# Kernel optimization log

Measured on AMD Instinct MI355X. Metric: run time of the kernel, lower is better.

Reference implementation:

```python
import jax, jax.numpy as jnp
import numpy as np

N, E = 50000, 800000
H_IN, H, L = 256, 128, 3
EPS = 1e-5  # BatchNorm1d default eps


def setup_inputs() -> dict:
    key = jax.random.key(0)
    ks = jax.random.split(key, 8)
    x = jax.random.normal(ks[0], (N, H_IN), jnp.float32)
    edge_index = jax.random.randint(ks[1], (2, E), 0, N, dtype=jnp.int32)

    def glorot(k, fi, fo):
        lim = np.sqrt(6.0 / (fi + fo)).astype(np.float32)
        return jax.random.uniform(k, (fi, fo), jnp.float32, -lim, lim)

    W_feat = glorot(ks[2], H_IN, H)
    b_feat = jnp.zeros((H,), jnp.float32)
    wkeys = jax.random.split(ks[3], L)
    Ws = jnp.stack([glorot(wkeys[i], H, H) for i in range(L)])
    bs = jnp.zeros((L, H), jnp.float32)
    # BN init per reset_parameters: weight=1, bias=1e-4
    bn_feat_g = jnp.ones((H_IN,), jnp.float32)
    bn_feat_b = jnp.full((H_IN,), 1e-4, jnp.float32)
    bn_g = jnp.ones((L, H), jnp.float32)
    bn_b = jnp.full((L, H), 1e-4, jnp.float32)
    return dict(x=x, edge_index=edge_index, bn_feat_g=bn_feat_g, bn_feat_b=bn_feat_b,
                W_feat=W_feat, b_feat=b_feat, bn_g=bn_g, bn_b=bn_b, Ws=Ws, bs=bs)


def _bn(x, gamma, beta):
    # training-mode BatchNorm1d: batch statistics over nodes, biased variance
    mu = x.mean(0)
    var = x.var(0)
    return (x - mu) * jax.lax.rsqrt(var + EPS) * gamma + beta


def _gcn_norm(edge_index, n):
    # add self-loops (fill value 1) + symmetric deg^-1/2 normalization
    row, col = edge_index[0], edge_index[1]
    loop = jnp.arange(n, dtype=row.dtype)
    row = jnp.concatenate([row, loop])
    col = jnp.concatenate([col, loop])
    deg = jax.ops.segment_sum(jnp.ones_like(row, jnp.float32), row, num_segments=n)
    dinv = jnp.where(deg > 0, jax.lax.rsqrt(deg), 0.0)
    return row, col, dinv[row] * dinv[col]


def _gcn(x, W, b, row, col, norm, n):
    x = x @ W                                   # [n, out]
    msg = x[row] * norm[:, None]                # gather + scale, [E+n, out]
    out = jax.ops.segment_sum(msg, col, num_segments=n)  # scatter-add
    return out + b


def reference(x, edge_index, bn_feat_g, bn_feat_b, W_feat, b_feat, bn_g, bn_b, Ws, bs):
    n = x.shape[0]
    row, col, norm = _gcn_norm(edge_index, n)   # same for every layer
    x = _bn(x, bn_feat_g, bn_feat_b)
    x = _gcn(x, W_feat, b_feat, row, col, norm, n)
    for i in range(L):
        x = _bn(x, bn_g[i], bn_b[i])
        x = _gcn(x, Ws[i], bs[i], row, col, norm, n)
    return x
```

## Files before the change

kernel.cpp:

```cpp
#include <hip/hip_runtime.h>
#include <hip/hip_bf16.h>

#define H_IN 256
#define H    128
#define BN_EPS 1e-5f
#define NCOPY 32
#define NSLICE 256
#define HSL 64
#define SMAX 5120
#define STATS_FLOATS (NCOPY * 2 * H_IN)
#define SBLK 1024
#define GEMMB 512

using u16 = unsigned short;
using u32 = unsigned int;
typedef __attribute__((ext_vector_type(8))) unsigned short us8;
typedef __attribute__((ext_vector_type(8))) short bf16x8;
typedef __attribute__((ext_vector_type(4))) float f32x4;

__device__ __forceinline__ float b2f(u16 u) {
    return __uint_as_float(((u32)u) << 16);
}
__device__ __forceinline__ u16 f2b(float f) {
    u32 u = __float_as_uint(f);
    u += 0x7FFF + ((u >> 16) & 1);
    return (u16)(u >> 16);
}

__global__ __launch_bounds__(256) void build_k(const int* __restrict__ row,
                                               const int* __restrict__ col,
                                               u32* __restrict__ hist_part,
                                               u32* __restrict__ bcnt_part,
                                               const float* __restrict__ x,
                                               u16* __restrict__ xb,
                                               float* __restrict__ statsA,
                                               int E, int total4, int QW, int qN) {
    extern __shared__ u32 smem[];
    int tid = threadIdx.x;
    int bx = blockIdx.x;
    if (bx < NSLICE) {
        u32* bcnt = smem;
        bcnt[tid] = 0;
        __syncthreads();
        int len = (E + NSLICE - 1) / NSLICE;
        int e0 = bx * len;
        int e1 = min(e0 + len, E);
        int e = e0 + tid;
        for (; e + 3 * 256 < e1; e += 4 * 256) {
            u32 c0 = (u32)col[e];
            u32 c1 = (u32)col[e + 256];
            u32 c2 = (u32)col[e + 512];
            u32 c3 = (u32)col[e + 768];
            atomicAdd(&bcnt[c0 >> 8], 1u);
            atomicAdd(&bcnt[c1 >> 8], 1u);
            atomicAdd(&bcnt[c2 >> 8], 1u);
            atomicAdd(&bcnt[c3 >> 8], 1u);
        }
        for (; e < e1; e += 256)
            atomicAdd(&bcnt[((u32)col[e]) >> 8], 1u);
        __syncthreads();
        bcnt_part[bx * 256 + tid] = bcnt[tid];
    } else if (bx < NSLICE + 4 * HSL) {
        int hb = bx - NSLICE;
        int s = hb >> 2;
        int qq = hb & 3;
        u32* hist = smem;
        for (int i = tid; i < QW; i += 256) hist[i] = 0;
        __syncthreads();
        int len = (E + HSL - 1) / HSL;
        int e0 = s * len;
        int e1 = min(e0 + len, E);
        int lo = qq * qN;
        int e = e0 + tid;
        for (; e + 3 * 256 < e1; e += 4 * 256) {
            int r0 = row[e] - lo;
            int r1 = row[e + 256] - lo;
            int r2 = row[e + 512] - lo;
            int r3 = row[e + 768] - lo;
            if ((u32)r0 < (u32)qN) atomicAdd(&hist[r0 >> 1], 1u << ((r0 & 1) << 4));
            if ((u32)r1 < (u32)qN) atomicAdd(&hist[r1 >> 1], 1u << ((r1 & 1) << 4));
            if ((u32)r2 < (u32)qN) atomicAdd(&hist[r2 >> 1], 1u << ((r2 & 1) << 4));
            if ((u32)r3 < (u32)qN) atomicAdd(&hist[r3 >> 1], 1u << ((r3 & 1) << 4));
        }
        for (; e < e1; e += 256) {
            int r = row[e] - lo;
            if ((u32)r < (u32)qN) atomicAdd(&hist[r >> 1], 1u << ((r & 1) << 4));
        }
        __syncthreads();
        u32* dst = hist_part + (size_t)hb * QW;
        for (int i = tid; i < QW; i += 256) dst[i] = hist[i];
    } else {
        float* sh = (float*)smem;
        const int K = H_IN;
        const int csz = 2 * H_IN;
        sh[tid] = 0.f;
        sh[tid + 256] = 0.f;
        __syncthreads();
        int sb = bx - NSLICE - 4 * HSL;
        int gid = sb * 256 + tid;
        int stride = SBLK * 256;
        int c0 = (tid * 4) & (H_IN - 1);
        float s0=0.f,s1=0.f,s2=0.f,s3=0.f, q0=0.f,q1=0.f,q2=0.f,q3=0.f;
        const float4* A4 = (const float4*)x;
        ushort4* X4 = (ushort4*)xb;
        auto proc = [&](int idx, float4 v) {
            ushort4 xv;
            xv.x = f2b(v.x); xv.y = f2b(v.y); xv.z = f2b(v.z); xv.w = f2b(v.w);
            X4[idx] = xv;
            s0 += v.x; q0 += v.x * v.x;
            s1 += v.y; q1 += v.y * v.y;
            s2 += v.z; q2 += v.z * v.z;
            s3 += v.w; q3 += v.w * v.w;
        };
        int i = gid;
        for (; i + 3 * stride < total4; i += 4 * stride) {
            float4 v0 = A4[i];
            float4 v1 = A4[i + stride];
            float4 v2 = A4[i + 2 * stride];
            float4 v3 = A4[i + 3 * stride];
            proc(i, v0);
            proc(i + stride, v1);
            proc(i + 2 * stride, v2);
            proc(i + 3 * stride, v3);
        }
        for (; i < total4; i += stride) proc(i, A4[i]);
        atomicAdd(&sh[c0],     s0); atomicAdd(&sh[K + c0],     q0);
        atomicAdd(&sh[c0 + 1], s1); atomicAdd(&sh[K + c0 + 1], q1);
        atomicAdd(&sh[c0 + 2], s2); atomicAdd(&sh[K + c0 + 2], q2);
        atomicAdd(&sh[c0 + 3], s3); atomicAdd(&sh[K + c0 + 3], q3);
        __syncthreads();
        float* dst = statsA + (size_t)(sb & (NCOPY - 1)) * csz;
        for (int i2 = tid; i2 < csz; i2 += 256) atomicAdd(&dst[i2], sh[i2]);
    }
}

__global__ __launch_bounds__(256) void prep_k(const int* __restrict__ row,
                                              const int* __restrict__ col,
                                              const u32* __restrict__ bcnt_part,
                                              u32* __restrict__ bbase,
                                              u32* __restrict__ ebuf,
                                              const u32* __restrict__ hist_part,
                                              float* __restrict__ dinv,
                                              const float* __restrict__ W,
                                              const float* __restrict__ stats_mc,
                                              const float* __restrict__ g,
                                              const float* __restrict__ bcoef,
                                              const float* __restrict__ bias,
                                              u16* __restrict__ Wt,
                                              float* __restrict__ bp,
                                              int E, int N, int DB, int QW, int qN) {
    int tid = threadIdx.x;
    int bx = blockIdx.x;
    if (bx < NSLICE) {
        __shared__ u32 sc[256];
        __shared__ u32 cur[256];
        int s = bx;
        u32 tot = 0, pre = 0;
        for (int t = 0; t < NSLICE; ++t) {
            u32 v = bcnt_part[t * 256 + tid];
            tot += v;
            if (t < s) pre += v;
        }
        sc[tid] = tot;
        __syncthreads();
        for (int o = 1; o < 256; o <<= 1) {
            u32 xv = (tid >= o) ? sc[tid - o] : 0;
            __syncthreads();
            sc[tid] += xv;
            __syncthreads();
        }
        u32 base = sc[tid] - tot;
        if (s == 0) {
            bbase[tid] = base;
            if (tid == 255) bbase[256] = sc[255];
        }
        cur[tid] = base + pre;
        __syncthreads();
        int len = (E + NSLICE - 1) / NSLICE;
        int e0 = s * len;
        int e1 = min(e0 + len, E);
        for (int e = e0 + tid; e < e1; e += 256) {
            u32 r = (u32)row[e];
            u32 c = (u32)col[e];
            u32 pos = atomicAdd(&cur[c >> 8], 1u);
            ebuf[pos] = r | ((c & 255u) << 16);
        }
    } else if (bx < NSLICE + DB) {
        int w = (bx - NSLICE) * 256 + tid;
        if (w < 4 * QW) {
            int qq = w / QW;
            int lw = w - qq * QW;
            u32 v = 0;
            for (int s = 0; s < HSL; ++s)
                v += hist_part[(size_t)(s * 4 + qq) * QW + lw];
            int n = qq * qN + 2 * lw;
            if (n < N)     dinv[n]     = rsqrtf((float)(v & 0xFFFF) + 1.0f);
            if (n + 1 < N) dinv[n + 1] = rsqrtf((float)(v >> 16) + 1.0f);
        }
    } else {
        int j = bx - NSLICE - DB;
        int k = tid;
        const int K = H_IN;
        const int csz = 2 * H_IN;
        float sum = 0.f, sumsq = 0.f;
#pragma unroll
        for (int c = 0; c < NCOPY; ++c) {
            sum   += stats_mc[(size_t)c * csz + k];
            sumsq += stats_mc[(size_t)c * csz + K + k];
        }
        float mu = sum / (float)N;
        float var = sumsq / (float)N - mu * mu;
        float sK = g[k] * rsqrtf(var + BN_EPS);
        float tK = bcoef[k] - mu * sK;
        float w = W[(size_t)k * H + j];
        Wt[(size_t)j * K + k] = f2b(sK * w);
        __shared__ float red[256];
        red[k] = tK * w;
        __syncthreads();
        for (int o = 128; o > 0; o >>= 1) {
            if (k < o) red[k] += red[k + o];
            __syncthreads();
        }
        if (k == 0) bp[j] = bias[j] + red[0];
    }
}

__global__ void fold_k(const float* __restrict__ W, const float* __restrict__ stats_mc,
                       const float* __restrict__ g, const float* __restrict__ b,
                       const float* __restrict__ bias, u16* __restrict__ Wt,
                       float* __restrict__ bp, int N, int K) {
    int j = blockIdx.x;
    int k = threadIdx.x;
    int csz = 2 * K;
    float sum = 0.f, sumsq = 0.f;
#pragma unroll
    for (int c = 0; c < NCOPY; ++c) {
        sum   += stats_mc[(size_t)c * csz + k];
        sumsq += stats_mc[(size_t)c * csz + K + k];
    }
    float mu = sum / (float)N;
    float var = sumsq / (float)N - mu * mu;
    float s = g[k] * rsqrtf(var + BN_EPS);
    float t = b[k] - mu * s;
    float w = W[(size_t)k * H + j];
    Wt[(size_t)j * K + k] = f2b(s * w);
    __shared__ float red[256];
    red[k] = t * w;
    __syncthreads();
    for (int o = blockDim.x >> 1; o > 0; o >>= 1) {
        if (k < o) red[k] += red[k + o];
        __syncthreads();
    }
    if (k == 0) bp[j] = bias[j] + red[0];
}

template<int KT, int WITH_SORT>
__global__ __launch_bounds__(256) void gemm_mfma_k(const u16* __restrict__ Ab,
                                                   const u16* __restrict__ Wt,
                                                   u16* __restrict__ Yb, int M,
                                                   float* __restrict__ stats_z,
                                                   const u32* __restrict__ ebuf,
                                                   const u32* __restrict__ bbase,
                                                   int* __restrict__ rowptr,
                                                   u16* __restrict__ esrc, int N) {
    int tid = threadIdx.x;
    if constexpr (WITH_SORT != 0) {
        if (blockIdx.x >= GEMMB) {
            __shared__ u32 est[SMAX];
            __shared__ u32 hist[256], scanv[256], cur[256];
            int b = blockIdx.x - GEMMB;
            u32 base = bbase[b];
            int size = (int)(bbase[b + 1] - base);
            int st = min(size, SMAX);
            hist[tid] = 0;
            __syncthreads();
            for (int i = tid; i < st; i += 256) {
                u32 e = ebuf[base + i];
                est[i] = e;
                atomicAdd(&hist[(e >> 16) & 255u], 1u);
            }
            for (int i = SMAX + tid; i < size; i += 256) {
                u32 e = ebuf[base + i];
                atomicAdd(&hist[(e >> 16) & 255u], 1u);
            }
            __syncthreads();
            u32 own = hist[tid];
            scanv[tid] = own;
            __syncthreads();
            for (int o = 1; o < 256; o <<= 1) {
                u32 t = (tid >= o) ? scanv[tid - o] : 0;
                __syncthreads();
                scanv[tid] += t;
                __syncthreads();
            }
            u32 excl = scanv[tid] - own;
            int idx = (b << 8) + tid;
            if (idx <= N) rowptr[idx] = (int)(base + excl);
            cur[tid] = excl;
            __syncthreads();
            for (int i = tid; i < st; i += 256) {
                u32 e = est[i];
                u32 pos = atomicAdd(&cur[(e >> 16) & 255u], 1u);
                esrc[base + pos] = (u16)(e & 0xFFFFu);
            }
            for (int i = SMAX + tid; i < size; i += 256) {
                u32 e = ebuf[base + i];
                u32 pos = atomicAdd(&cur[(e >> 16) & 255u], 1u);
                esrc[base + pos] = (u16)(e & 0xFFFFu);
            }
            return;
        }
    }
    const int K = KT * 32;
    if (stats_z && blockIdx.x == 0) {
        for (int i = tid; i < STATS_FLOATS; i += 256) stats_z[i] = 0.f;
    }
    int w = tid >> 6;
    int lane = tid & 63;
    int m16 = lane & 15;
    int q = lane >> 4;

    bf16x8 bfrag[KT][2];
#pragma unroll
    for (int t = 0; t < KT; ++t)
#pragma unroll
        for (int p = 0; p < 2; ++p) {
            int ncol = 32 * w + 16 * p + m16;
            bfrag[t][p] = *(const bf16x8*)(Wt + (size_t)ncol * K + 32 * t + 8 * q);
        }

    int nchunk = M >> 4;
    for (int c = blockIdx.x; c < nchunk; c += GEMMB) {
        int m0 = c << 4;
        const u16* Arow = Ab + (size_t)(m0 + m16) * K + 8 * q;
        bf16x8 afrag[KT];
#pragma unroll
        for (int t = 0; t < KT; ++t)
            afrag[t] = *(const bf16x8*)(Arow + 32 * t);
        f32x4 acc0 = {0.f, 0.f, 0.f, 0.f}, acc1 = {0.f, 0.f, 0.f, 0.f};
#pragma unroll
        for (int t = 0; t < KT; ++t) {
            acc0 = __builtin_amdgcn_mfma_f32_16x16x32_bf16(afrag[t], bfrag[t][0], acc0, 0, 0, 0);
            acc1 = __builtin_amdgcn_mfma_f32_16x16x32_bf16(afrag[t], bfrag[t][1], acc1, 0, 0, 0);
        }
        u16* Crow = Yb + (size_t)(m0 + q * 4) * H + 32 * w + m16;
#pragma unroll
        for (int i = 0; i < 4; ++i) {
            Crow[(size_t)i * H]      = f2b(acc0[i]);
            Crow[(size_t)i * H + 16] = f2b(acc1[i]);
        }
    }
}

__global__ __launch_bounds__(256) void csragg_k(const int* __restrict__ rowptr,
                                                const u16* __restrict__ esrc,
                                                const u16* __restrict__ Yb,
                                                const float* __restrict__ dinv,
                                                const float* __restrict__ bp,
                                                u16* __restrict__ Ob,
                                                float* __restrict__ Of,
                                                float* __restrict__ stats_mc,
                                                int do_stats, int N) {
    __shared__ float sh[1024];
    int tid = threadIdx.x;
    int node = blockIdx.x * 16 + (tid >> 4);
    int fl = tid & 15;
    float o[8] = {0.f,0.f,0.f,0.f,0.f,0.f,0.f,0.f};
    if (node < N) {
        const us8* Y8 = (const us8*)Yb;
        float dn = dinv[node];
        float acc[8];
        {
            us8 ys = Y8[(size_t)node * 16 + fl];
#pragma unroll
            for (int j = 0; j < 8; ++j) acc[j] = dn * b2f(ys[j]);
        }
        int s = rowptr[node], e = rowptr[node + 1];
        int p = s;
        for (; p + 3 < e; p += 4) {
            int s0 = esrc[p], s1 = esrc[p + 1], s2 = esrc[p + 2], s3 = esrc[p + 3];
            float n0 = dinv[s0], n1 = dinv[s1], n2 = dinv[s2], n3 = dinv[s3];
            us8 v0 = Y8[(size_t)s0 * 16 + fl];
            us8 v1 = Y8[(size_t)s1 * 16 + fl];
            us8 v2 = Y8[(size_t)s2 * 16 + fl];
            us8 v3 = Y8[(size_t)s3 * 16 + fl];
#pragma unroll
            for (int j = 0; j < 8; ++j) acc[j] += n0 * b2f(v0[j]);
#pragma unroll
            for (int j = 0; j < 8; ++j) acc[j] += n1 * b2f(v1[j]);
#pragma unroll
            for (int j = 0; j < 8; ++j) acc[j] += n2 * b2f(v2[j]);
#pragma unroll
            for (int j = 0; j < 8; ++j) acc[j] += n3 * b2f(v3[j]);
        }
        for (; p < e; ++p) {
            int s0 = esrc[p];
            float n0 = dinv[s0];
            us8 v0 = Y8[(size_t)s0 * 16 + fl];
#pragma unroll
            for (int j = 0; j < 8; ++j) acc[j] += n0 * b2f(v0[j]);
        }
        float4 b0 = ((const float4*)bp)[fl * 2];
        float4 b1 = ((const float4*)bp)[fl * 2 + 1];
        o[0] = b0.x + dn * acc[0]; o[1] = b0.y + dn * acc[1];
        o[2] = b0.z + dn * acc[2]; o[3] = b0.w + dn * acc[3];
        o[4] = b1.x + dn * acc[4]; o[5] = b1.y + dn * acc[5];
        o[6] = b1.z + dn * acc[6]; o[7] = b1.w + dn * acc[7];
        if (Of) {
            float4* O4 = (float4*)Of;
            O4[(size_t)node * 32 + fl * 2]     = make_float4(o[0], o[1], o[2], o[3]);
            O4[(size_t)node * 32 + fl * 2 + 1] = make_float4(o[4], o[5], o[6], o[7]);
        } else {
            us8 ov;
#pragma unroll
            for (int j = 0; j < 8; ++j) ov[j] = f2b(o[j]);
            *(us8*)(Ob + (size_t)node * H + fl * 8) = ov;
        }
    }
    if (do_stats) {
        float sv[16];
#pragma unroll
        for (int j = 0; j < 8; ++j) { sv[j] = o[j]; sv[8 + j] = o[j] * o[j]; }
#pragma unroll
        for (int j = 0; j < 16; ++j) {
            sv[j] += __shfl_xor(sv[j], 16, 64);
            sv[j] += __shfl_xor(sv[j], 32, 64);
        }
        int lane = tid & 63, wv = tid >> 6;
        if (lane < 16) {
            float* base = sh + wv * 256;
#pragma unroll
            for (int j = 0; j < 8; ++j) {
                base[fl * 8 + j]       = sv[j];
                base[128 + fl * 8 + j] = sv[8 + j];
            }
        }
        __syncthreads();
        float v = sh[tid] + sh[256 + tid] + sh[512 + tid] + sh[768 + tid];
        atomicAdd(&stats_mc[(size_t)(blockIdx.x & (NCOPY - 1)) * (2 * H) + tid], v);
    }
}

extern "C" void kernel_launch(void* const* d_in, const int* in_sizes, int n_in,
                              void* d_out, int out_size, void* d_ws, size_t ws_size,
                              hipStream_t stream) {
    const float* x     = (const float*)d_in[0];
    const int*   ei    = (const int*)d_in[1];
    const float* bnfg  = (const float*)d_in[2];
    const float* bnfb  = (const float*)d_in[3];
    const float* Wfeat = (const float*)d_in[4];
    const float* bfeat = (const float*)d_in[5];
    const float* bng   = (const float*)d_in[6];
    const float* bnb   = (const float*)d_in[7];
    const float* Ws    = (const float*)d_in[8];
    const float* bs    = (const float*)d_in[9];

    int N = in_sizes[0] / H_IN;
    int E = in_sizes[1] / 2;
    const int* row = ei;
    const int* col = ei + E;

    int NB = (N + 255) >> 8;
    int QW = (N + 7) / 8;
    int qN = 2 * QW;
    int DB = (4 * QW + 255) / 256;

    char* p = (char*)d_ws;
    auto alloc = [&](size_t bytes) { char* r = p; p += (bytes + 63) & ~size_t(63); return r; };
    float* statsA    = (float*)alloc(STATS_FLOATS * 4);
    float* statsB    = (float*)alloc(STATS_FLOATS * 4);
    float* dinv      = (float*)alloc((size_t)N * 4);
    u16*   Wt        = (u16*)alloc(H_IN * H * 2);
    float* bp        = (float*)alloc(H * 4);
    u32*   hist_part = (u32*)alloc((size_t)4 * HSL * QW * 4);
    u32*   bcnt_part = (u32*)alloc(NSLICE * 256 * 4);
    u32*   bbase     = (u32*)alloc(257 * 4);
    int*   rowptr    = (int*)alloc((size_t)(N + 1) * 4);
    u32*   ebuf      = (u32*)alloc((size_t)E * 4);
    u16*   esrc      = (u16*)alloc((size_t)E * 2);
    u16*   xb        = (u16*)alloc((size_t)N * H_IN * 2);
    u16*   Yb        = (u16*)alloc((size_t)N * H * 2);
    u16*   ACTb      = (u16*)alloc((size_t)N * H * 2);

    float* out = (float*)d_out;

    hipMemsetAsync(statsA, 0, (size_t)(2 * STATS_FLOATS) * 4, stream);

    size_t lds_bytes = (size_t)QW * 4;
    if (lds_bytes < 2 * H_IN * 4) lds_bytes = 2 * H_IN * 4;

    build_k<<<NSLICE + 4 * HSL + SBLK, 256, lds_bytes, stream>>>(row, col, hist_part,
                                                                 bcnt_part, x, xb, statsA,
                                                                 E, N * H_IN / 4, QW, qN);
    prep_k<<<NSLICE + DB + H, 256, 0, stream>>>(row, col, bcnt_part, bbase, ebuf,
                                                hist_part, dinv,
                                                Wfeat, statsA, bnfg, bnfb, bfeat, Wt, bp,
                                                E, N, DB, QW, qN);
    gemm_mfma_k<8, 1><<<GEMMB + NB, 256, 0, stream>>>(xb, Wt, Yb, N, nullptr,
                                                      ebuf, bbase, rowptr, esrc, N);
    csragg_k<<<(N + 15) / 16, 256, 0, stream>>>(rowptr, esrc, Yb, dinv, bp,
                                                ACTb, nullptr, statsB, 1, N);

    for (int l = 1; l < 4; ++l) {
        const float* W    = Ws + (size_t)(l - 1) * H * H;
        const float* bias = bs + (size_t)(l - 1) * H;
        const float* g    = bng + (size_t)(l - 1) * H;
        const float* bb   = bnb + (size_t)(l - 1) * H;
        float* sfold   = (l & 1) ? statsB : statsA;
        float* szero   = (l == 1) ? statsA : (l == 2) ? statsB : nullptr;
        float* starget = ((l + 1) & 1) ? statsB : statsA;

        fold_k<<<H, H, 0, stream>>>(W, sfold, g, bb, bias, Wt, bp, N, H);
        gemm_mfma_k<4, 0><<<GEMMB, 256, 0, stream>>>(ACTb, Wt, Yb, N, szero,
                                                     nullptr, nullptr, nullptr, nullptr, N);
        csragg_k<<<(N + 15) / 16, 256, 0, stream>>>(rowptr, esrc, Yb, dinv, bp,
                                                    ACTb, (l == 3) ? out : nullptr,
                                                    starget, (l < 3) ? 1 : 0, N);
    }
}
```

Measured before the change: 340.6 us.

## Fuse BN weight folding into GEMM and sub-sort CSR edges by source chunk

Result: no change. 344.1 us, median of 2 (+1.0%).

```diff
diff --git a/kernel.cpp b/kernel.cpp
--- a/kernel.cpp
+++ b/kernel.cpp
@@ -11,6 +11,8 @@
 #define STATS_FLOATS (NCOPY * 2 * H_IN)
 #define SBLK 1024
 #define GEMMB 512
+#define CH_SH 13
+#define NBIN 2048
 
 using u16 = unsigned short;
 using u32 = unsigned int;
@@ -156,7 +158,17 @@
         __shared__ u32 cur[256];
         int s = bx;
         u32 tot = 0, pre = 0;
-        for (int t = 0; t < NSLICE; ++t) {
+        int t = 0;
+        for (; t + 3 < NSLICE; t += 4) {
+            u32 v0 = bcnt_part[(t    ) * 256 + tid];
+            u32 v1 = bcnt_part[(t + 1) * 256 + tid];
+            u32 v2 = bcnt_part[(t + 2) * 256 + tid];
+            u32 v3 = bcnt_part[(t + 3) * 256 + tid];
+            tot += v0 + v1 + v2 + v3;
+            pre += (t < s ? v0 : 0) + (t + 1 < s ? v1 : 0) +
+                   (t + 2 < s ? v2 : 0) + (t + 3 < s ? v3 : 0);
+        }
+        for (; t < NSLICE; ++t) {
             u32 v = bcnt_part[t * 256 + tid];
             tot += v;
             if (t < s) pre += v;
@@ -225,36 +237,7 @@
     }
 }
 
-__global__ void fold_k(const float* __restrict__ W, const float* __restrict__ stats_mc,
-                       const float* __restrict__ g, const float* __restrict__ b,
-                       const float* __restrict__ bias, u16* __restrict__ Wt,
-                       float* __restrict__ bp, int N, int K) {
-    int j = blockIdx.x;
-    int k = threadIdx.x;
-    int csz = 2 * K;
-    float sum = 0.f, sumsq = 0.f;
-#pragma unroll
-    for (int c = 0; c < NCOPY; ++c) {
-        sum   += stats_mc[(size_t)c * csz + k];
-        sumsq += stats_mc[(size_t)c * csz + K + k];
-    }
-    float mu = sum / (float)N;
-    float var = sumsq / (float)N - mu * mu;
-    float s = g[k] * rsqrtf(var + BN_EPS);
-    float t = b[k] - mu * s;
-    float w = W[(size_t)k * H + j];
-    Wt[(size_t)j * K + k] = f2b(s * w);
-    __shared__ float red[256];
-    red[k] = t * w;
-    __syncthreads();
-    for (int o = blockDim.x >> 1; o > 0; o >>= 1) {
-        if (k < o) red[k] += red[k + o];
-        __syncthreads();
-    }
-    if (k == 0) bp[j] = bias[j] + red[0];
-}
-
-template<int KT, int WITH_SORT>
+template<int KT, int WITH_SORT, int FOLD>
 __global__ __launch_bounds__(256) void gemm_mfma_k(const u16* __restrict__ Ab,
                                                    const u16* __restrict__ Wt,
                                                    u16* __restrict__ Yb, int M,
@@ -262,56 +245,101 @@
                                                    const u32* __restrict__ ebuf,
                                                    const u32* __restrict__ bbase,
                                                    int* __restrict__ rowptr,
-                                                   u16* __restrict__ esrc, int N) {
+                                                   u16* __restrict__ esrc, int N,
+                                                   const float* __restrict__ Wf,
+                                                   const float* __restrict__ stats_mc,
+                                                   const float* __restrict__ g,
+                                                   const float* __restrict__ bb,
+                                                   const float* __restrict__ bias,
+                                                   float* __restrict__ bp) {
     int tid = threadIdx.x;
+    __shared__ u16 wt[FOLD ? H : 1][136];
     if constexpr (WITH_SORT != 0) {
         if (blockIdx.x >= GEMMB) {
             __shared__ u32 est[SMAX];
-            __shared__ u32 hist[256], scanv[256], cur[256];
+            __shared__ u32 hist[NBIN], cur[NBIN];
+            __shared__ u32 scanw[256];
             int b = blockIdx.x - GEMMB;
             u32 base = bbase[b];
             int size = (int)(bbase[b + 1] - base);
             int st = min(size, SMAX);
-            hist[tid] = 0;
+            for (int i = tid; i < NBIN; i += 256) hist[i] = 0;
             __syncthreads();
             for (int i = tid; i < st; i += 256) {
                 u32 e = ebuf[base + i];
                 est[i] = e;
-                atomicAdd(&hist[(e >> 16) & 255u], 1u);
+                u32 bin = (((e >> 16) & 255u) << 3) | ((e & 0xFFFFu) >> CH_SH);
+                atomicAdd(&hist[bin], 1u);
             }
             for (int i = SMAX + tid; i < size; i += 256) {
                 u32 e = ebuf[base + i];
-                atomicAdd(&hist[(e >> 16) & 255u], 1u);
-            }
-            __syncthreads();
-            u32 own = hist[tid];
-            scanv[tid] = own;
+                u32 bin = (((e >> 16) & 255u) << 3) | ((e & 0xFFFFu) >> CH_SH);
+                atomicAdd(&hist[bin], 1u);
+            }
+            __syncthreads();
+            u32 loc[8];
+            u32 run = 0;
+#pragma unroll
+            for (int i = 0; i < 8; ++i) { loc[i] = run; run += hist[tid * 8 + i]; }
+            scanw[tid] = run;
             __syncthreads();
             for (int o = 1; o < 256; o <<= 1) {
-                u32 t = (tid >= o) ? scanv[tid - o] : 0;
+                u32 t2 = (tid >= o) ? scanw[tid - o] : 0;
                 __syncthreads();
-                scanv[tid] += t;
+                scanw[tid] += t2;
                 __syncthreads();
             }
-            u32 excl = scanv[tid] - own;
+            u32 off = scanw[tid] - run;
             int idx = (b << 8) + tid;
-            if (idx <= N) rowptr[idx] = (int)(base + excl);
-            cur[tid] = excl;
+            if (idx <= N) rowptr[idx] = (int)(base + off);
+#pragma unroll
+            for (int i = 0; i < 8; ++i) cur[tid * 8 + i] = off + loc[i];
             __syncthreads();
             for (int i = tid; i < st; i += 256) {
                 u32 e = est[i];
-                u32 pos = atomicAdd(&cur[(e >> 16) & 255u], 1u);
+                u32 bin = (((e >> 16) & 255u) << 3) | ((e & 0xFFFFu) >> CH_SH);
+                u32 pos = atomicAdd(&cur[bin], 1u);
                 esrc[base + pos] = (u16)(e & 0xFFFFu);
             }
             for (int i = SMAX + tid; i < size; i += 256) {
                 u32 e = ebuf[base + i];
-                u32 pos = atomicAdd(&cur[(e >> 16) & 255u], 1u);
+                u32 bin = (((e >> 16) & 255u) << 3) | ((e & 0xFFFFu) >> CH_SH);
+                u32 pos = atomicAdd(&cur[bin], 1u);
                 esrc[base + pos] = (u16)(e & 0xFFFFu);
             }
             return;
         }
     }
     const int K = KT * 32;
+    if constexpr (FOLD != 0) {
+        __shared__ float s_sh[H], t_sh[H];
+        __shared__ float red2[256];
+        if (tid < H) {
+            float sum = 0.f, sumsq = 0.f;
+#pragma unroll
+            for (int c = 0; c < NCOPY; ++c) {
+                sum   += stats_mc[(size_t)c * (2 * H) + tid];
+                sumsq += stats_mc[(size_t)c * (2 * H) + H + tid];
+            }
+            float mu = sum / (float)N;
+            float var = sumsq / (float)N - mu * mu;
+            float sv = g[tid] * rsqrtf(var + BN_EPS);
+            s_sh[tid] = sv;
+            t_sh[tid] = bb[tid] - mu * sv;
+        }
+        __syncthreads();
+        int j = tid & 127, half = tid >> 7;
+        float bpacc = 0.f;
+        for (int it = 0; it < 64; ++it) {
+            int k = it * 2 + half;
+            float w = Wf[(size_t)k * H + j];
+            wt[j][k] = f2b(s_sh[k] * w);
+            bpacc += t_sh[k] * w;
+        }
+        red2[tid] = bpacc;
+        __syncthreads();
+        if (blockIdx.x == 0 && tid < H) bp[tid] = bias[tid] + red2[tid] + red2[tid + 128];
+    }
     if (stats_z && blockIdx.x == 0) {
         for (int i = tid; i < STATS_FLOATS; i += 256) stats_z[i] = 0.f;
     }
@@ -326,7 +354,10 @@
 #pragma unroll
         for (int p = 0; p < 2; ++p) {
             int ncol = 32 * w + 16 * p + m16;
-            bfrag[t][p] = *(const bf16x8*)(Wt + (size_t)ncol * K + 32 * t + 8 * q);
+            if constexpr (FOLD != 0)
+                bfrag[t][p] = *(const bf16x8*)(&wt[ncol][32 * t + 8 * q]);
+            else
+                bfrag[t][p] = *(const bf16x8*)(Wt + (size_t)ncol * K + 32 * t + 8 * q);
         }
 
     int nchunk = M >> 4;
@@ -496,8 +527,10 @@
                                                 hist_part, dinv,
                                                 Wfeat, statsA, bnfg, bnfb, bfeat, Wt, bp,
                                                 E, N, DB, QW, qN);
-    gemm_mfma_k<8, 1><<<GEMMB + NB, 256, 0, stream>>>(xb, Wt, Yb, N, nullptr,
-                                                      ebuf, bbase, rowptr, esrc, N);
+    gemm_mfma_k<8, 1, 0><<<GEMMB + NB, 256, 0, stream>>>(xb, Wt, Yb, N, nullptr,
+                                                         ebuf, bbase, rowptr, esrc, N,
+                                                         nullptr, nullptr, nullptr,
+                                                         nullptr, nullptr, nullptr);
     csragg_k<<<(N + 15) / 16, 256, 0, stream>>>(rowptr, esrc, Yb, dinv, bp,
                                                 ACTb, nullptr, statsB, 1, N);
 
@@ -510,9 +543,9 @@
         float* szero   = (l == 1) ? statsA : (l == 2) ? statsB : nullptr;
         float* starget = ((l + 1) & 1) ? statsB : statsA;
 
-        fold_k<<<H, H, 0, stream>>>(W, sfold, g, bb, bias, Wt, bp, N, H);
-        gemm_mfma_k<4, 0><<<GEMMB, 256, 0, stream>>>(ACTb, Wt, Yb, N, szero,
-                                                     nullptr, nullptr, nullptr, nullptr, N);
+        gemm_mfma_k<4, 0, 1><<<GEMMB, 256, 0, stream>>>(ACTb, nullptr, Yb, N, szero,
+                                                        nullptr, nullptr, nullptr, nullptr, N,
+                                                        W, sfold, g, bb, bias, bp);
         csragg_k<<<(N + 15) / 16, 256, 0, stream>>>(rowptr, esrc, Yb, dinv, bp,
                                                     ACTb, (l == 3) ? out : nullptr,
                                                     starget, (l < 3) ? 1 : 0, N);
```
